# Kernel tuning notes

Measured on AMD Instinct MI355X. Metric: run time of the kernel, lower is better.

Reference implementation:

```python
import jax, jax.numpy as jnp
import numpy as np

D_MODEL = 1024


def setup_inputs() -> dict:
    key = jax.random.key(0)
    ks = jax.random.split(key, 8)
    B, S, D = 2, 2048, D_MODEL
    s = 1.0 / np.sqrt(D)
    causal = jnp.where(jnp.tril(jnp.ones((S, S), dtype=bool)), 0.0, -1e9)[None, None]
    return {
        "query": jax.random.normal(ks[0], (B, S, D), jnp.float32),
        "key": jax.random.normal(ks[1], (B, S, D), jnp.float32),
        "value": jax.random.normal(ks[2], (B, S, D), jnp.float32),
        "padding_mask": jnp.zeros((B, 1, 1, S), jnp.float32),
        "lookahead_mask": causal.astype(jnp.float32),
        "w_q": jax.random.normal(ks[3], (D, D), jnp.float32) * s,
        "w_k": jax.random.normal(ks[4], (D, D), jnp.float32) * s,
        "w_v": jax.random.normal(ks[5], (D, D), jnp.float32) * s,
        "w_out": jax.random.normal(ks[6], (D, D), jnp.float32) * s,
        "b_q": jnp.zeros((D,), jnp.float32),
        "b_k": jnp.zeros((D,), jnp.float32),
        "b_v": jnp.zeros((D,), jnp.float32),
        "b_out": jnp.zeros((D,), jnp.float32),
        "n_heads": 16,
    }


def reference(query, key, value, padding_mask, lookahead_mask,
              w_q, w_k, w_v, w_out, b_q, b_k, b_v, b_out, n_heads):
    B, S, D = query.shape
    d_k = D // n_heads
    # projections (torch Linear: x @ W.T + b; here weights stored as (in, out))
    q = (query @ w_q + b_q).reshape(B, S, n_heads, d_k).transpose(0, 2, 1, 3)
    k = (key @ w_k + b_k).reshape(B, S, n_heads, d_k).transpose(0, 2, 1, 3)
    v = (value @ w_v + b_v).reshape(B, S, n_heads, d_k).transpose(0, 2, 1, 3)
    scores = jnp.einsum("bhqd,bhkd->bhqk", q, k) / jnp.sqrt(jnp.float32(d_k))
    scores = scores + padding_mask + lookahead_mask
    attn = jax.nn.softmax(scores, axis=-1)
    out = jnp.einsum("bhqk,bhkd->bhqd", attn, v)
    out = out.transpose(0, 2, 1, 3).reshape(B, S, D)
    return out @ w_out + b_out
```

## Files before the change

kernel.cpp:

```cpp
#include <hip/hip_runtime.h>
#include <hip/hip_bf16.h>
#include <stdint.h>

typedef __bf16 bf16x8 __attribute__((ext_vector_type(8)));
typedef __bf16 bf16x4 __attribute__((ext_vector_type(4)));
typedef float f32x4 __attribute__((ext_vector_type(4)));

#define DMODEL 1024
#define SEQ    2048
#define NHEAD  16
#define DK     64
#define MTOT   4096
#define KDIM   1024

#define DRAIN_VM_LGKM() asm volatile("s_waitcnt vmcnt(0) lgkmcnt(0)" ::: "memory")
#define DRAIN_LGKM()    asm volatile("s_waitcnt lgkmcnt(0)" ::: "memory")

__device__ __forceinline__ void gl2lds16(const void* g, void* l) {
  __builtin_amdgcn_global_load_lds((__attribute__((address_space(1))) void*)(g),
                                   (__attribute__((address_space(3))) void*)(l),
                                   16, 0, 0);
}

__global__ __launch_bounds__(256) void k_cvt3(const float* __restrict__ q,
                                              const float* __restrict__ k,
                                              const float* __restrict__ v,
                                              __bf16* __restrict__ oq,
                                              __bf16* __restrict__ ok,
                                              __bf16* __restrict__ ov,
                                              int n4) {
  const int which = blockIdx.y;
  const float* in = which == 0 ? q : (which == 1 ? k : v);
  __bf16* out = which == 0 ? oq : (which == 1 ? ok : ov);
  const int i = blockIdx.x * 256 + threadIdx.x;
  if (i >= n4) return;
  const float4 f = ((const float4*)in)[i];
  bf16x4 o = { (__bf16)f.x, (__bf16)f.y, (__bf16)f.z, (__bf16)f.w };
  ((bf16x4*)out)[i] = o;
}

__global__ __launch_bounds__(256) void k_transpose4(const float* __restrict__ w0,
                                                    const float* __restrict__ w1,
                                                    const float* __restrict__ w2,
                                                    const float* __restrict__ w3,
                                                    __bf16* __restrict__ t0,
                                                    __bf16* __restrict__ t1,
                                                    __bf16* __restrict__ t2,
                                                    __bf16* __restrict__ t3) {
  const int z = blockIdx.z;
  const float* W = z == 0 ? w0 : (z == 1 ? w1 : (z == 2 ? w2 : w3));
  __bf16* WT = z == 0 ? t0 : (z == 1 ? t1 : (z == 2 ? t2 : t3));
  __shared__ float tile[32][33];
  int n0 = blockIdx.x * 32, k0 = blockIdx.y * 32;
  int tx = threadIdx.x & 31, ty = threadIdx.x >> 5;
  #pragma unroll
  for (int i = ty; i < 32; i += 8)
    tile[i][tx] = W[(size_t)(k0 + i) * DMODEL + n0 + tx];
  __syncthreads();
  #pragma unroll
  for (int i = ty; i < 32; i += 8)
    WT[(size_t)(n0 + i) * DMODEL + k0 + tx] = (__bf16)tile[tx][i];
}

__global__ __launch_bounds__(256) void k_gemm_qkv(
    const __bf16* __restrict__ A0, const __bf16* __restrict__ A1, const __bf16* __restrict__ A2,
    const __bf16* __restrict__ W0, const __bf16* __restrict__ W1, const __bf16* __restrict__ W2,
    const float* __restrict__ bi0, const float* __restrict__ bi1, const float* __restrict__ bi2,
    __bf16* __restrict__ C0, __bf16* __restrict__ C1, __bf16* __restrict__ C2) {
  const int z = blockIdx.z;
  const __bf16* A  = z == 0 ? A0 : (z == 1 ? A1 : A2);
  const __bf16* BT = z == 0 ? W0 : (z == 1 ? W1 : W2);
  const float* bias = z == 0 ? bi0 : (z == 1 ? bi1 : bi2);
  __bf16* Cout = z == 0 ? C0 : (z == 1 ? C1 : C2);

  __shared__ __align__(16) __bf16 As[128 * 32];
  __shared__ __align__(16) __bf16 Bs[128 * 32];
  const int tid = threadIdx.x;
  const int lane = tid & 63;
  const int wv = tid >> 6;
  const int wm = wv >> 1, wn = wv & 1;
  const int m0 = blockIdx.y * 128, n0 = blockIdx.x * 128;
  const int lr = lane & 15, lg = lane >> 4;

  f32x4 acc[4][4] = {};

  for (int k0 = 0; k0 < KDIM; k0 += 32) {
    #pragma unroll
    for (int i = 0; i < 2; ++i) {
      int c = tid + i * 256;
      int row = c >> 2, seg = c & 3;
      gl2lds16(A + (size_t)(m0 + row) * KDIM + k0 + seg * 8, (char*)As + c * 16);
      gl2lds16(BT + (size_t)(n0 + row) * KDIM + k0 + seg * 8, (char*)Bs + c * 16);
    }
    DRAIN_VM_LGKM();
    __syncthreads();
    bf16x8 af[4], bfr[4];
    #pragma unroll
    for (int mi = 0; mi < 4; ++mi)
      af[mi] = *(const bf16x8*)&As[(wm * 64 + mi * 16 + lr) * 32 + lg * 8];
    #pragma unroll
    for (int ni = 0; ni < 4; ++ni)
      bfr[ni] = *(const bf16x8*)&Bs[(wn * 64 + ni * 16 + lr) * 32 + lg * 8];
    #pragma unroll
    for (int mi = 0; mi < 4; ++mi)
      #pragma unroll
      for (int ni = 0; ni < 4; ++ni)
        acc[mi][ni] = __builtin_amdgcn_mfma_f32_16x16x32_bf16(af[mi], bfr[ni], acc[mi][ni], 0, 0, 0);
    DRAIN_LGKM();
    __syncthreads();
  }

  #pragma unroll
  for (int mi = 0; mi < 4; ++mi)
    #pragma unroll
    for (int ni = 0; ni < 4; ++ni) {
      const int col = n0 + wn * 64 + ni * 16 + lr;
      const float bv = bias[col];
      #pragma unroll
      for (int r = 0; r < 4; ++r) {
        const int row = m0 + wm * 64 + mi * 16 + lg * 4 + r;
        float v = acc[mi][ni][r] + bv;
        const int b = row >> 11, s = row & (SEQ - 1);
        const int h = col >> 6, dd = col & (DK - 1);
        if (z == 2)
          Cout[((size_t)(b * NHEAD + h) * DK + dd) * SEQ + s] = (__bf16)v;
        else
          Cout[((size_t)(b * NHEAD + h) * SEQ + s) * DK + dd] = (__bf16)v;
      }
    }
}

__global__ __launch_bounds__(256) void k_gemm_out(const __bf16* __restrict__ A,
                                                  const __bf16* __restrict__ BT,
                                                  const float* __restrict__ bias,
                                                  float* __restrict__ Cout) {
  __shared__ __align__(16) __bf16 As[128 * 32];
  __shared__ __align__(16) __bf16 Bs[128 * 32];
  const int tid = threadIdx.x;
  const int lane = tid & 63;
  const int wv = tid >> 6;
  const int wm = wv >> 1, wn = wv & 1;
  const int m0 = blockIdx.y * 128, n0 = blockIdx.x * 128;
  const int lr = lane & 15, lg = lane >> 4;

  f32x4 acc[4][4] = {};

  for (int k0 = 0; k0 < KDIM; k0 += 32) {
    #pragma unroll
    for (int i = 0; i < 2; ++i) {
      int c = tid + i * 256;
      int row = c >> 2, seg = c & 3;
      gl2lds16(A + (size_t)(m0 + row) * KDIM + k0 + seg * 8, (char*)As + c * 16);
      gl2lds16(BT + (size_t)(n0 + row) * KDIM + k0 + seg * 8, (char*)Bs + c * 16);
    }
    DRAIN_VM_LGKM();
    __syncthreads();
    bf16x8 af[4], bfr[4];
    #pragma unroll
    for (int mi = 0; mi < 4; ++mi)
      af[mi] = *(const bf16x8*)&As[(wm * 64 + mi * 16 + lr) * 32 + lg * 8];
    #pragma unroll
    for (int ni = 0; ni < 4; ++ni)
      bfr[ni] = *(const bf16x8*)&Bs[(wn * 64 + ni * 16 + lr) * 32 + lg * 8];
    #pragma unroll
    for (int mi = 0; mi < 4; ++mi)
      #pragma unroll
      for (int ni = 0; ni < 4; ++ni)
        acc[mi][ni] = __builtin_amdgcn_mfma_f32_16x16x32_bf16(af[mi], bfr[ni], acc[mi][ni], 0, 0, 0);
    DRAIN_LGKM();
    __syncthreads();
  }

  #pragma unroll
  for (int mi = 0; mi < 4; ++mi)
    #pragma unroll
    for (int ni = 0; ni < 4; ++ni) {
      const int col = n0 + wn * 64 + ni * 16 + lr;
      const float bv = bias[col];
      #pragma unroll
      for (int r = 0; r < 4; ++r) {
        const int row = m0 + wm * 64 + mi * 16 + lg * 4 + r;
        Cout[(size_t)row * DMODEL + col] = acc[mi][ni][r] + bv;
      }
    }
}

__global__ __launch_bounds__(256, 2) void k_attn(const __bf16* __restrict__ Q,
                                                 const __bf16* __restrict__ Kt,
                                                 const __bf16* __restrict__ Vt,
                                                 const float* __restrict__ pmask,
                                                 __bf16* __restrict__ O) {
  __shared__ __align__(16) __bf16 Ks[2][128 * 64];
  __shared__ __align__(16) __bf16 Vs[2][64 * 128];
  __shared__ __align__(16) __bf16 plds[4][16 * 128];

  const int tid = threadIdx.x;
  const int lane = tid & 63, wv = tid >> 6;
  const int lr = lane & 15, lg = lane >> 4;

  const int bid = blockIdx.x;
  const int xcd = bid & 7;
  const int rdec = bid >> 3;
  const int slot = rdec >> 4;
  const int pair = rdec & 15;
  const int bh = slot * 8 + xcd;
  const int b = bh >> 4, h = bh & 15;

  const __bf16* Qb = Q + (size_t)bh * SEQ * DK;
  const __bf16* Kb = Kt + (size_t)bh * SEQ * DK;
  const __bf16* Vb = Vt + (size_t)bh * DK * SEQ;
  const float* pm = pmask + (size_t)b * SEQ;
  const float SCL = 0.125f * 1.44269504f;
  const float L2E = 1.44269504f;

  auto stage = [&](int buf, int t) {
    #pragma unroll
    for (int i = 0; i < 4; ++i) {
      const int c = tid + i * 256;
      const int row = c >> 3;
      const int sx = ((c & 7) * 16) ^ ((row & 7) << 4);
      gl2lds16((const char*)Kb + (size_t)(t * 128 + row) * 128 + sx,
               (char*)&Ks[buf][0] + c * 16);
    }
    #pragma unroll
    for (int i = 0; i < 4; ++i) {
      const int c = tid + i * 256;
      const int row = c >> 4;
      const int sx = ((c & 15) * 16) ^ ((row & 7) << 4);
      gl2lds16((const char*)Vb + (size_t)row * (SEQ * 2) + (size_t)t * 256 + sx,
               (char*)&Vs[buf][0] + c * 16);
    }
  };

  for (int half = 0; half < 2; ++half) {
    const int qb = half ? (31 - pair) : pair;
    const int nt = (qb + 2) >> 1;
    const int QR = qb * 64 + wv * 16;

    const bf16x8 qf0 = *(const bf16x8*)&Qb[(size_t)(QR + lr) * DK + lg * 8];
    const bf16x8 qf1 = *(const bf16x8*)&Qb[(size_t)(QR + lr) * DK + 32 + lg * 8];

    float mrow = -1e30f, lrw = 0.f;
    f32x4 oacc[4] = {};

    stage(0, 0);
    DRAIN_VM_LGKM();
    __syncthreads();
    int cur = 0;
    for (int t = 0; t < nt; ++t) {
      if (t + 1 < nt) stage(cur ^ 1, t + 1);
      f32x4 sc[8];
      #pragma unroll
      for (int g = 0; g < 8; ++g) {
        const int krow = g * 16 + lr;
        const int ksw = (lr & 7) << 4;
        bf16x8 kf0 = *(const bf16x8*)((const char*)&Ks[cur][0] + krow * 128 + ((lg * 16) ^ ksw));
        bf16x8 kf1 = *(const bf16x8*)((const char*)&Ks[cur][0] + krow * 128 + ((64 + lg * 16) ^ ksw));
        f32x4 a = {};
        a = __builtin_amdgcn_mfma_f32_16x16x32_bf16(kf0, qf0, a, 0, 0, 0);
        a = __builtin_amdgcn_mfma_f32_16x16x32_bf16(kf1, qf1, a, 0, 0, 0);
        sc[g] = a;
      }
      const bool edge = (t == nt - 1);
      #pragma unroll
      for (int g = 0; g < 8; ++g) {
        const float4 pmv = *(const float4*)&pm[t * 128 + g * 16 + lg * 4];
        const float pmf[4] = {pmv.x, pmv.y, pmv.z, pmv.w};
        #pragma unroll
        for (int r = 0; r < 4; ++r) {
          float s = sc[g][r] * SCL + pmf[r] * L2E;
          if (edge && (t * 128 + g * 16 + lg * 4 + r > QR + lr)) s = -1e30f;
          sc[g][r] = s;
        }
      }
      float pmax = sc[0][0];
      #pragma unroll
      for (int g = 0; g < 8; ++g)
        #pragma unroll
        for (int r = 0; r < 4; ++r) pmax = fmaxf(pmax, sc[g][r]);
      pmax = fmaxf(pmax, __shfl_xor(pmax, 16, 64));
      pmax = fmaxf(pmax, __shfl_xor(pmax, 32, 64));
      if (!__all(pmax <= mrow + 8.f)) {
        const float mnew = fmaxf(mrow, pmax);
        const float alpha = exp2f(mrow - mnew);
        mrow = mnew;
        lrw *= alpha;
        #pragma unroll
        for (int r = 0; r < 4; ++r) {
          const float av = __shfl(alpha, lg * 4 + r, 64);
          #pragma unroll
          for (int og = 0; og < 4; ++og) oacc[og][r] *= av;
        }
      }
      float psum = 0.f;
      #pragma unroll
      for (int g = 0; g < 8; ++g)
        #pragma unroll
        for (int r = 0; r < 4; ++r) {
          float p = exp2f(sc[g][r] - mrow);
          sc[g][r] = p;
          psum += p;
        }
      psum += __shfl_xor(psum, 16, 64);
      psum += __shfl_xor(psum, 32, 64);
      lrw += psum;
      #pragma unroll
      for (int g = 0; g < 8; ++g) {
        bf16x4 pk = { (__bf16)sc[g][0], (__bf16)sc[g][1], (__bf16)sc[g][2], (__bf16)sc[g][3] };
        const int byteoff = lr * 256 + ((g * 32 + lg * 8) ^ ((lr & 7) << 4));
        *(bf16x4*)((char*)plds[wv] + byteoff) = pk;
      }
      #pragma unroll
      for (int kk = 0; kk < 4; ++kk) {
        const int pboff = lr * 256 + ((kk * 64 + lg * 16) ^ ((lr & 7) << 4));
        const bf16x8 pa = *(const bf16x8*)((char*)plds[wv] + pboff);
        #pragma unroll
        for (int og = 0; og < 4; ++og) {
          const int vrow = og * 16 + lr;
          const bf16x8 vf = *(const bf16x8*)((const char*)&Vs[cur][0] + vrow * 256 + ((kk * 64 + lg * 16) ^ ((lr & 7) << 4)));
          oacc[og] = __builtin_amdgcn_mfma_f32_16x16x32_bf16(pa, vf, oacc[og], 0, 0, 0);
        }
      }
      DRAIN_VM_LGKM();
      __syncthreads();
      cur ^= 1;
    }

    #pragma unroll
    for (int r = 0; r < 4; ++r) {
      const float lsh = __shfl(lrw, lg * 4 + r, 64);
      const float inv = 1.f / lsh;
      const int row = QR + lg * 4 + r;
      #pragma unroll
      for (int og = 0; og < 4; ++og)
        O[((size_t)b * SEQ + row) * DMODEL + h * DK + og * 16 + lr] = (__bf16)(oacc[og][r] * inv);
    }
  }
}

extern "C" void kernel_launch(void* const* d_in, const int* in_sizes, int n_in,
                              void* d_out, int out_size, void* d_ws, size_t ws_size,
                              hipStream_t stream) {
  (void)in_sizes; (void)n_in; (void)out_size; (void)ws_size;
  const float* query = (const float*)d_in[0];
  const float* key   = (const float*)d_in[1];
  const float* value = (const float*)d_in[2];
  const float* pmask = (const float*)d_in[3];
  const float* w_q = (const float*)d_in[5];
  const float* w_k = (const float*)d_in[6];
  const float* w_v = (const float*)d_in[7];
  const float* w_o = (const float*)d_in[8];
  const float* b_q = (const float*)d_in[9];
  const float* b_k = (const float*)d_in[10];
  const float* b_v = (const float*)d_in[11];
  const float* b_o = (const float*)d_in[12];

  __bf16* ws = (__bf16*)d_ws;
  const size_t WSZ = (size_t)DMODEL * DMODEL;
  const size_t XSZ = (size_t)MTOT * DMODEL;
  __bf16* WTq = ws;
  __bf16* WTk = WTq + WSZ;
  __bf16* WTv = WTk + WSZ;
  __bf16* WTo = WTv + WSZ;
  __bf16* Xq  = WTo + WSZ;
  __bf16* Xk  = Xq + XSZ;
  __bf16* Xv  = Xk + XSZ;
  __bf16* Qh  = Xv + XSZ;
  __bf16* Kh  = Qh + XSZ;
  __bf16* Vh  = Kh + XSZ;
  __bf16* Oh  = Xq;

  dim3 blk(256);
  k_cvt3<<<dim3(4096, 3), blk, 0, stream>>>(query, key, value, Xq, Xk, Xv, (int)(XSZ / 4));
  k_transpose4<<<dim3(32, 32, 4), blk, 0, stream>>>(w_q, w_k, w_v, w_o, WTq, WTk, WTv, WTo);

  k_gemm_qkv<<<dim3(8, 32, 3), blk, 0, stream>>>(Xq, Xk, Xv, WTq, WTk, WTv,
                                                 b_q, b_k, b_v, Qh, Kh, Vh);

  k_attn<<<dim3(512), blk, 0, stream>>>(Qh, Kh, Vh, pmask, Oh);

  k_gemm_out<<<dim3(8, 32), blk, 0, stream>>>(Oh, WTo, b_o, (float*)d_out);
}
```

Baseline: 145.4 us.

## Fuse fp32-to-bf16 input conversion into QKV GEMM, widen K tile, add MFMA priority

Removes the separate conversion kernel and has the QKV GEMM load fp32 activations directly into registers, convert them to bf16 and write them to LDS, with the next tile's A loads issued before the MFMAs. Both GEMMs move from a K step of 32 to 64, halving the barrier count, and the QKV GEMM gets an occupancy hint. The attention kernel raises wave priority around its MFMA sections. The aim is to drop one launch and the intermediate bf16 round-trip through memory. In exchange the QKV GEMM needs more registers and reads twice the A bytes per tile.

Result: slower. 159.9 us (+10.0%).

```diff
diff --git a/kernel.cpp b/kernel.cpp
--- a/kernel.cpp
+++ b/kernel.cpp
@@ -20,23 +20,6 @@
   __builtin_amdgcn_global_load_lds((__attribute__((address_space(1))) void*)(g),
                                    (__attribute__((address_space(3))) void*)(l),
                                    16, 0, 0);
-}
-
-__global__ __launch_bounds__(256) void k_cvt3(const float* __restrict__ q,
-                                              const float* __restrict__ k,
-                                              const float* __restrict__ v,
-                                              __bf16* __restrict__ oq,
-                                              __bf16* __restrict__ ok,
-                                              __bf16* __restrict__ ov,
-                                              int n4) {
-  const int which = blockIdx.y;
-  const float* in = which == 0 ? q : (which == 1 ? k : v);
-  __bf16* out = which == 0 ? oq : (which == 1 ? ok : ov);
-  const int i = blockIdx.x * 256 + threadIdx.x;
-  if (i >= n4) return;
-  const float4 f = ((const float4*)in)[i];
-  bf16x4 o = { (__bf16)f.x, (__bf16)f.y, (__bf16)f.z, (__bf16)f.w };
-  ((bf16x4*)out)[i] = o;
 }
 
 __global__ __launch_bounds__(256) void k_transpose4(const float* __restrict__ w0,
@@ -62,19 +45,19 @@
     WT[(size_t)(n0 + i) * DMODEL + k0 + tx] = (__bf16)tile[tx][i];
 }
 
-__global__ __launch_bounds__(256) void k_gemm_qkv(
-    const __bf16* __restrict__ A0, const __bf16* __restrict__ A1, const __bf16* __restrict__ A2,
+__global__ __launch_bounds__(256, 3) void k_gemm_qkv(
+    const float* __restrict__ A0, const float* __restrict__ A1, const float* __restrict__ A2,
     const __bf16* __restrict__ W0, const __bf16* __restrict__ W1, const __bf16* __restrict__ W2,
     const float* __restrict__ bi0, const float* __restrict__ bi1, const float* __restrict__ bi2,
     __bf16* __restrict__ C0, __bf16* __restrict__ C1, __bf16* __restrict__ C2) {
   const int z = blockIdx.z;
-  const __bf16* A  = z == 0 ? A0 : (z == 1 ? A1 : A2);
+  const float* A   = z == 0 ? A0 : (z == 1 ? A1 : A2);
   const __bf16* BT = z == 0 ? W0 : (z == 1 ? W1 : W2);
   const float* bias = z == 0 ? bi0 : (z == 1 ? bi1 : bi2);
   __bf16* Cout = z == 0 ? C0 : (z == 1 ? C1 : C2);
 
-  __shared__ __align__(16) __bf16 As[128 * 32];
-  __shared__ __align__(16) __bf16 Bs[128 * 32];
+  __shared__ __align__(16) __bf16 As[128 * 64];
+  __shared__ __align__(16) __bf16 Bs[128 * 64];
   const int tid = threadIdx.x;
   const int lane = tid & 63;
   const int wv = tid >> 6;
@@ -83,29 +66,56 @@
   const int lr = lane & 15, lg = lane >> 4;
 
   f32x4 acc[4][4] = {};
-
-  for (int k0 = 0; k0 < KDIM; k0 += 32) {
-    #pragma unroll
-    for (int i = 0; i < 2; ++i) {
-      int c = tid + i * 256;
-      int row = c >> 2, seg = c & 3;
-      gl2lds16(A + (size_t)(m0 + row) * KDIM + k0 + seg * 8, (char*)As + c * 16);
+  float4 ar[8];
+
+  auto loadA = [&](int k0) {
+    #pragma unroll
+    for (int i = 0; i < 4; ++i) {
+      const int c = tid + i * 256;
+      const int row = c >> 3, seg = c & 7;
+      const float* p = A + (size_t)(m0 + row) * KDIM + k0 + seg * 8;
+      ar[i * 2]     = *(const float4*)p;
+      ar[i * 2 + 1] = *(const float4*)(p + 4);
+    }
+  };
+  auto writeA = [&]() {
+    #pragma unroll
+    for (int i = 0; i < 4; ++i) {
+      const int c = tid + i * 256;
+      const float4 f0 = ar[i * 2], f1 = ar[i * 2 + 1];
+      bf16x8 v = { (__bf16)f0.x, (__bf16)f0.y, (__bf16)f0.z, (__bf16)f0.w,
+                   (__bf16)f1.x, (__bf16)f1.y, (__bf16)f1.z, (__bf16)f1.w };
+      *(bf16x8*)((char*)As + c * 16) = v;
+    }
+  };
+
+  loadA(0);
+  for (int k0 = 0; k0 < KDIM; k0 += 64) {
+    #pragma unroll
+    for (int i = 0; i < 4; ++i) {
+      const int c = tid + i * 256;
+      const int row = c >> 3, seg = c & 7;
       gl2lds16(BT + (size_t)(n0 + row) * KDIM + k0 + seg * 8, (char*)Bs + c * 16);
     }
+    writeA();
     DRAIN_VM_LGKM();
     __syncthreads();
-    bf16x8 af[4], bfr[4];
-    #pragma unroll
-    for (int mi = 0; mi < 4; ++mi)
-      af[mi] = *(const bf16x8*)&As[(wm * 64 + mi * 16 + lr) * 32 + lg * 8];
-    #pragma unroll
-    for (int ni = 0; ni < 4; ++ni)
-      bfr[ni] = *(const bf16x8*)&Bs[(wn * 64 + ni * 16 + lr) * 32 + lg * 8];
-    #pragma unroll
-    for (int mi = 0; mi < 4; ++mi)
+    if (k0 + 64 < KDIM) loadA(k0 + 64);
+    #pragma unroll
+    for (int hh = 0; hh < 2; ++hh) {
+      bf16x8 af[4], bfr[4];
+      #pragma unroll
+      for (int mi = 0; mi < 4; ++mi)
+        af[mi] = *(const bf16x8*)&As[(wm * 64 + mi * 16 + lr) * 64 + hh * 32 + lg * 8];
       #pragma unroll
       for (int ni = 0; ni < 4; ++ni)
-        acc[mi][ni] = __builtin_amdgcn_mfma_f32_16x16x32_bf16(af[mi], bfr[ni], acc[mi][ni], 0, 0, 0);
+        bfr[ni] = *(const bf16x8*)&Bs[(wn * 64 + ni * 16 + lr) * 64 + hh * 32 + lg * 8];
+      #pragma unroll
+      for (int mi = 0; mi < 4; ++mi)
+        #pragma unroll
+        for (int ni = 0; ni < 4; ++ni)
+          acc[mi][ni] = __builtin_amdgcn_mfma_f32_16x16x32_bf16(af[mi], bfr[ni], acc[mi][ni], 0, 0, 0);
+    }
     DRAIN_LGKM();
     __syncthreads();
   }
@@ -134,8 +144,8 @@
                                                   const __bf16* __restrict__ BT,
                                                   const float* __restrict__ bias,
                                                   float* __restrict__ Cout) {
-  __shared__ __align__(16) __bf16 As[128 * 32];
-  __shared__ __align__(16) __bf16 Bs[128 * 32];
+  __shared__ __align__(16) __bf16 As[128 * 64];
+  __shared__ __align__(16) __bf16 Bs[128 * 64];
   const int tid = threadIdx.x;
   const int lane = tid & 63;
   const int wv = tid >> 6;
@@ -145,28 +155,31 @@
 
   f32x4 acc[4][4] = {};
 
-  for (int k0 = 0; k0 < KDIM; k0 += 32) {
-    #pragma unroll
-    for (int i = 0; i < 2; ++i) {
-      int c = tid + i * 256;
-      int row = c >> 2, seg = c & 3;
+  for (int k0 = 0; k0 < KDIM; k0 += 64) {
+    #pragma unroll
+    for (int i = 0; i < 4; ++i) {
+      const int c = tid + i * 256;
+      const int row = c >> 3, seg = c & 7;
       gl2lds16(A + (size_t)(m0 + row) * KDIM + k0 + seg * 8, (char*)As + c * 16);
       gl2lds16(BT + (size_t)(n0 + row) * KDIM + k0 + seg * 8, (char*)Bs + c * 16);
     }
     DRAIN_VM_LGKM();
     __syncthreads();
-    bf16x8 af[4], bfr[4];
-    #pragma unroll
-    for (int mi = 0; mi < 4; ++mi)
-      af[mi] = *(const bf16x8*)&As[(wm * 64 + mi * 16 + lr) * 32 + lg * 8];
-    #pragma unroll
-    for (int ni = 0; ni < 4; ++ni)
-      bfr[ni] = *(const bf16x8*)&Bs[(wn * 64 + ni * 16 + lr) * 32 + lg * 8];
-    #pragma unroll
-    for (int mi = 0; mi < 4; ++mi)
+    #pragma unroll
+    for (int hh = 0; hh < 2; ++hh) {
+      bf16x8 af[4], bfr[4];
+      #pragma unroll
+      for (int mi = 0; mi < 4; ++mi)
+        af[mi] = *(const bf16x8*)&As[(wm * 64 + mi * 16 + lr) * 64 + hh * 32 + lg * 8];
       #pragma unroll
       for (int ni = 0; ni < 4; ++ni)
-        acc[mi][ni] = __builtin_amdgcn_mfma_f32_16x16x32_bf16(af[mi], bfr[ni], acc[mi][ni], 0, 0, 0);
+        bfr[ni] = *(const bf16x8*)&Bs[(wn * 64 + ni * 16 + lr) * 64 + hh * 32 + lg * 8];
+      #pragma unroll
+      for (int mi = 0; mi < 4; ++mi)
+        #pragma unroll
+        for (int ni = 0; ni < 4; ++ni)
+          acc[mi][ni] = __builtin_amdgcn_mfma_f32_16x16x32_bf16(af[mi], bfr[ni], acc[mi][ni], 0, 0, 0);
+    }
     DRAIN_LGKM();
     __syncthreads();
   }
@@ -250,6 +263,7 @@
     for (int t = 0; t < nt; ++t) {
       if (t + 1 < nt) stage(cur ^ 1, t + 1);
       f32x4 sc[8];
+      __builtin_amdgcn_s_setprio(1);
       #pragma unroll
       for (int g = 0; g < 8; ++g) {
         const int krow = g * 16 + lr;
@@ -261,6 +275,7 @@
         a = __builtin_amdgcn_mfma_f32_16x16x32_bf16(kf1, qf1, a, 0, 0, 0);
         sc[g] = a;
       }
+      __builtin_amdgcn_s_setprio(0);
       const bool edge = (t == nt - 1);
       #pragma unroll
       for (int g = 0; g < 8; ++g) {
@@ -310,6 +325,7 @@
         const int byteoff = lr * 256 + ((g * 32 + lg * 8) ^ ((lr & 7) << 4));
         *(bf16x4*)((char*)plds[wv] + byteoff) = pk;
       }
+      __builtin_amdgcn_s_setprio(1);
       #pragma unroll
       for (int kk = 0; kk < 4; ++kk) {
         const int pboff = lr * 256 + ((kk * 64 + lg * 16) ^ ((lr & 7) << 4));
@@ -321,6 +337,7 @@
           oacc[og] = __builtin_amdgcn_mfma_f32_16x16x32_bf16(pa, vf, oacc[og], 0, 0, 0);
         }
       }
+      __builtin_amdgcn_s_setprio(0);
       DRAIN_VM_LGKM();
       __syncthreads();
       cur ^= 1;
@@ -362,19 +379,15 @@
   __bf16* WTk = WTq + WSZ;
   __bf16* WTv = WTk + WSZ;
   __bf16* WTo = WTv + WSZ;
-  __bf16* Xq  = WTo + WSZ;
-  __bf16* Xk  = Xq + XSZ;
-  __bf16* Xv  = Xk + XSZ;
-  __bf16* Qh  = Xv + XSZ;
+  __bf16* Qh  = WTo + WSZ;
   __bf16* Kh  = Qh + XSZ;
   __bf16* Vh  = Kh + XSZ;
-  __bf16* Oh  = Xq;
+  __bf16* Oh  = Vh + XSZ;
 
   dim3 blk(256);
-  k_cvt3<<<dim3(4096, 3), blk, 0, stream>>>(query, key, value, Xq, Xk, Xv, (int)(XSZ / 4));
   k_transpose4<<<dim3(32, 32, 4), blk, 0, stream>>>(w_q, w_k, w_v, w_o, WTq, WTk, WTv, WTo);
 
-  k_gemm_qkv<<<dim3(8, 32, 3), blk, 0, stream>>>(Xq, Xk, Xv, WTq, WTk, WTv,
+  k_gemm_qkv<<<dim3(8, 32, 3), blk, 0, stream>>>(query, key, value, WTq, WTk, WTv,
                                                  b_q, b_k, b_v, Qh, Kh, Vh);
 
   k_attn<<<dim3(512), blk, 0, stream>>>(Qh, Kh, Vh, pmask, Oh);
```
